# Kernel optimization log

Hardware: AMD Instinct MI355X
Metric: run time of the kernel (lower is better)

## Reference

```python
import jax, jax.numpy as jnp
import numpy as np
from jax import lax

NMODES, STEP, DTAPS, NTAPS = 2, 5, 1001, 101
HID = 100
L_FIBER = 2000000.0
DZ = L_FIBER / STEP
GAMMA = 0.0016567
D_PARAM = 16.5
FC = 299792458.0 / 1.55e-6
FS_NOM = 160e9
B, SEQ = 4, 500000


def _get_beta2(D, Fc):
    c_kms = 299792458.0 / 1e3  # speed of light [km/s]
    lamb = c_kms / Fc          # wavelength [km]
    return -(D * lamb ** 2) / (2.0 * np.pi * c_kms)


def _dispersion_kernel(Fs):
    # Fs: [B] sampling rate in Hz -> time-domain dispersion kernel [B, DTAPS] complex64
    beta2 = _get_beta2(D_PARAM, FC) / 1000.0  # [s^2/m]
    beta1 = 0.0  # Fi == Fc so the walk-off term vanishes
    dz = -DZ     # module calls dispersion_kernel(-self.dz, ...)
    f = np.fft.fftfreq(DTAPS).astype(np.float32)
    omega = 2.0 * np.pi * Fs[:, None] * f  # [B, DTAPS] rad/s
    phase = (beta2 / 2.0) * omega ** 2 * dz + beta1 * omega * dz
    kf = jnp.exp(-1j * phase)  # freq-domain response, complex64
    return jnp.fft.fftshift(jnp.fft.ifft(kf, axis=-1), axes=-1).astype(jnp.complex64)


def _nonlinear_kernel(task_info, W1, b1, W2, b2):
    # hypernetwork-generated nonlinear kernel [B, NMODES, NMODES, NTAPS]
    scale = 1.0 / 200.0
    b = task_info.shape[0]
    Fs = task_info[:, 2] / FS_NOM
    Ts = (1.0 / Fs)[:, None, None]  # [B,1,1] (broadcasts over taps like expand)
    pos = jnp.abs(jnp.arange(-(NTAPS // 2), NTAPS // 2 + 1)).astype(jnp.float32)
    pos = pos[None, :, None] * scale  # [1,NTAPS,1]
    inp = pos * Ts ** 2               # [B,NTAPS,1]
    h = jax.nn.relu(inp @ W1 + b1)    # [B,NTAPS,HID]
    mlp_out = h @ W2 + b2             # [B,NTAPS,NMODES^2]
    k1 = Ts ** 2 * mlp_out * jnp.exp(-pos * Ts ** 2)
    return jnp.transpose(k1, (0, 2, 1)).reshape(b, NMODES, NMODES, NTAPS)


def _corr(x, h):
    # x:[B,M,L] real, h:[B,taps] -> valid cross-correlation [B,M,L-taps+1] (torch conv1d semantics)
    def one(xb, hb):
        return lax.conv_general_dilated(xb[:, None, :], hb[None, None, :], (1,), 'VALID')[:, 0]
    return jax.vmap(one)(x, h)


def _nconv(p, K):
    # p:[B,Min,L], K:[B,Mout,Min,taps] -> [B,Mout,L-taps+1]
    def one(pb, Kb):
        return lax.conv_general_dilated(pb[None], Kb, (1,), 'VALID')[0]
    return jax.vmap(one)(p, K)


def _forward(x_real, x_imag, task_info, W1, b1, W2, b2):
    P = 0.001 * 10.0 ** (task_info[:, 0] / 10.0) / NMODES  # launch power per mode [W]
    Dk = _dispersion_kernel(task_info[:, 2])
    hr, hi = jnp.real(Dk), jnp.imag(Dk)
    Nk = _nonlinear_kernel(task_info, W1, b1, W2, b2)
    xr = jnp.transpose(x_real, (0, 2, 1))  # [B,M,L]
    xi = jnp.transpose(x_imag, (0, 2, 1))
    trim = (NTAPS - 1) // 2
    coef = (GAMMA * DZ) * P[:, None, None]
    for _ in range(STEP):
        # complex dispersion conv: (xr+i xi) * (hr+i hi)
        ar = _corr(xr, hr) - _corr(xi, hi)
        ai = _corr(xr, hi) + _corr(xi, hr)
        # nonlinear phase from |x|^2 filtered by hypernet kernel
        phi = _nconv(ar ** 2 + ai ** 2, Nk)  # [B,M,L-ntaps+1]
        theta = phi * coef
        c, s = jnp.cos(theta), jnp.sin(theta)
        art = ar[:, :, trim:ar.shape[2] - trim]
        ait = ai[:, :, trim:ai.shape[2] - trim]
        # x * exp(i*theta)
        xr = art * c - ait * s
        xi = art * s + ait * c
    out = jnp.stack([xr, xi], axis=-1)      # [B,M,Lout,2]
    return jnp.transpose(out, (0, 2, 1, 3))  # [B,Lout,M,2] (real/imag stacked)


def setup_inputs() -> dict:
    key = jax.random.key(0)
    k = jax.random.split(key, 6)
    x_real = jax.random.normal(k[0], (B, SEQ, NMODES), jnp.float32)
    x_imag = jax.random.normal(k[1], (B, SEQ, NMODES), jnp.float32)
    Pdbm = jax.random.uniform(k[2], (B,), jnp.float32, -2.0, 2.0)
    task_info = jnp.stack([Pdbm,
                           jnp.full((B,), FC, jnp.float32),
                           jnp.full((B,), FS_NOM, jnp.float32),
                           jnp.ones((B,), jnp.float32)], axis=1)
    W1 = jax.random.normal(k[3], (1, HID), jnp.float32) * 0.5
    b1 = jnp.zeros((HID,), jnp.float32)
    W2 = jax.random.normal(k[4], (HID, NMODES * NMODES), jnp.float32) * 0.02
    b2 = jnp.zeros((NMODES * NMODES,), jnp.float32)
    return {"x_real": x_real, "x_imag": x_imag, "task_info": task_info,
            "W1": W1, "b1": b1, "W2": W2, "b2": b2}


def reference(x_real, x_imag, task_info, W1, b1, W2, b2):
    return _forward(x_real, x_imag, task_info, W1, b1, W2, b2)
```

## Files before the change

### kernel.cpp

```cpp
#include <hip/hip_runtime.h>

#define NM      2
#define STEPS_C 5
#define DTAPS_C 1001
#define NTAPS_C 101
#define HID_C   100
#define B_C     4
#define SEQ_C   500000
#define SSTR    SEQ_C
#define NKP     104
#define FS_NOM_D 160000000000.0
#define PI_D 3.14159265358979323846

#define SWZ(L) ((L) + ((((unsigned)(L)) >> 5) << 2))

#define LD4V(A0,A1,A2,A3, SRC) { float4 q_ = *(const float4*)&(SRC); \
    A0=q_.x; A1=q_.y; A2=q_.z; A3=q_.w; }

__global__ void build_disp(const float* __restrict__ task,
                           float* __restrict__ HR, float* __restrict__ HI)
{
    __shared__ double skr[DTAPS_C], ski[DTAPS_C];
    const int b = blockIdx.y;
    const double Fs = (double)task[b * 4 + 2];
    const double c_kms = 299792458.0 / 1000.0;
    const double Fc    = 299792458.0 / 1.55e-6;
    const double lamb  = c_kms / Fc;
    const double beta2 = -(16.5 * lamb * lamb) / (2.0 * PI_D * c_kms) / 1000.0;
    const double dz    = -400000.0;

    for (int k = threadIdx.x; k < DTAPS_C; k += blockDim.x) {
        double fk = ((k <= DTAPS_C / 2) ? (double)k : (double)(k - DTAPS_C)) / (double)DTAPS_C;
        double om = 2.0 * PI_D * Fs * fk;
        double ph = 0.5 * beta2 * om * om * dz;
        ph = fmod(ph, 2.0 * PI_D);
        double s, c; sincos(ph, &s, &c);
        skr[k] = c;  ski[k] = -s;
    }
    __syncthreads();

    const int ln = threadIdx.x >> 3;
    const int kp = threadIdx.x & 7;
    const int n  = blockIdx.x * 32 + ln;
    double dr = 0.0, di = 0.0;
    {
        const int nn = (n < DTAPS_C) ? n : 0;
        const int r0 = (nn * kp) % DTAPS_C;
        const int rs = (nn * 8) % DTAPS_C;
        double a0 = 2.0 * PI_D * (double)r0 / (double)DTAPS_C;
        double as = 2.0 * PI_D * (double)rs / (double)DTAPS_C;
        double s0, c0, ss, cs;
        sincos(a0, &s0, &c0);
        sincos(as, &ss, &cs);
        for (int k = kp; k < DTAPS_C; k += 8) {
            dr += skr[k] * c0 - ski[k] * s0;
            di += skr[k] * s0 + ski[k] * c0;
            const double nc = c0 * cs - s0 * ss;
            s0 = c0 * ss + s0 * cs;
            c0 = nc;
        }
    }
    #pragma unroll
    for (int m = 1; m <= 4; m <<= 1) {
        dr += __shfl_xor(dr, m, 64);
        di += __shfl_xor(di, m, 64);
    }
    if (kp == 0 && n < DTAPS_C) {
        int m = n + DTAPS_C / 2; if (m >= DTAPS_C) m -= DTAPS_C;
        HR[b * DTAPS_C + m] = (float)(dr / (double)DTAPS_C);
        HI[b * DTAPS_C + m] = (float)(di / (double)DTAPS_C);
    }
}

__global__ void build_G(const float* __restrict__ HR, const float* __restrict__ HI,
                        float* __restrict__ Gb)
{
    __shared__ float shr[DTAPS_C], shi[DTAPS_C];
    const int b = blockIdx.y;
    for (int k = threadIdx.x; k < DTAPS_C; k += blockDim.x) {
        shr[k] = HR[b * DTAPS_C + k];
        shi[k] = HI[b * DTAPS_C + k];
    }
    __syncthreads();

    const int ln = threadIdx.x >> 3;
    const int kp = threadIdx.x & 7;
    const int f  = blockIdx.x * 32 + ln;
    double ar = 0.0, ai = 0.0;
    {
        const int r0 = (f * kp) & 4095;
        const int rs = (f * 8) & 4095;
        double a0 = (2.0 * PI_D / 4096.0) * (double)r0;
        double as = (2.0 * PI_D / 4096.0) * (double)rs;
        double s0, c0, ss, cs;
        sincos(a0, &s0, &c0);
        sincos(as, &ss, &cs);
        for (int k = kp; k < DTAPS_C; k += 8) {
            const double hre = (double)shr[k], him = (double)shi[k];
            ar += hre * c0 - him * s0;
            ai += hre * s0 + him * c0;
            const double nc = c0 * cs - s0 * ss;
            s0 = c0 * ss + s0 * cs;
            c0 = nc;
        }
    }
    #pragma unroll
    for (int m = 1; m <= 4; m <<= 1) {
        ar += __shfl_xor(ar, m, 64);
        ai += __shfl_xor(ai, m, 64);
    }
    if (kp == 0) {
        const int p = ((f & 15) << 8) + (((f >> 4) & 15) << 4) + (f >> 8);
        Gb[(size_t)(b * 4096 + p) * 2 + 0] = (float)(ar * (1.0 / 4096.0));
        Gb[(size_t)(b * 4096 + p) * 2 + 1] = (float)(ai * (1.0 / 4096.0));
    }
}

__global__ void build_nk(const float* __restrict__ task,
                         const float* __restrict__ W1, const float* __restrict__ b1,
                         const float* __restrict__ W2, const float* __restrict__ b2,
                         float* __restrict__ NKg, float* __restrict__ COEF)
{
    const int tid = threadIdx.x;
    for (int i = tid; i < B_C * 4 * NKP; i += blockDim.x) NKg[i] = 0.f;
    if (tid < B_C) {
        float pdbm = task[tid * 4 + 0];
        float P = 0.001f * powf(10.f, pdbm * 0.1f) / (float)NM;
        COEF[tid] = (float)(0.0016567 * 400000.0) * P;
    }
    __syncthreads();
    if (tid < B_C * NTAPS_C) {
        const int b = tid / NTAPS_C, tap = tid % NTAPS_C;
        float Fsn = task[b * 4 + 2] * (float)(1.0 / FS_NOM_D);
        float Ts = 1.f / Fsn, Ts2 = Ts * Ts;
        float pos = fabsf((float)(tap - NTAPS_C / 2)) * (1.f / 200.f);
        float inp = pos * Ts2;
        float o0 = b2[0], o1 = b2[1], o2 = b2[2], o3 = b2[3];
        for (int j = 0; j < HID_C; ++j) {
            float h = fmaxf(fmaf(inp, W1[j], b1[j]), 0.f);
            o0 = fmaf(h, W2[j * 4 + 0], o0);
            o1 = fmaf(h, W2[j * 4 + 1], o1);
            o2 = fmaf(h, W2[j * 4 + 2], o2);
            o3 = fmaf(h, W2[j * 4 + 3], o3);
        }
        float sc = Ts2 * expf(-pos * Ts2);
        NKg[(b * 4 + 0) * NKP + tap] = o0 * sc;
        NKg[(b * 4 + 1) * NKP + tap] = o1 * sc;
        NKg[(b * 4 + 2) * NKP + tap] = o2 * sc;
        NKg[(b * 4 + 3) * NKP + tap] = o3 * sc;
    }
}

__global__ void transpose_in(const float* __restrict__ xr_in, const float* __restrict__ xi_in,
                             float* __restrict__ XR, float* __restrict__ XI)
{
    int idx = blockIdx.x * blockDim.x + threadIdx.x;
    if (idx >= B_C * SEQ_C) return;
    int b = idx / SEQ_C, t = idx - b * SEQ_C;
    float2 vr = ((const float2*)xr_in)[idx];
    float2 vi = ((const float2*)xi_in)[idx];
    XR[(size_t)(b * 2 + 0) * SSTR + t] = vr.x;
    XR[(size_t)(b * 2 + 1) * SSTR + t] = vr.y;
    XI[(size_t)(b * 2 + 0) * SSTR + t] = vi.x;
    XI[(size_t)(b * 2 + 1) * SSTR + t] = vi.y;
}

template<int SGN>
__device__ __forceinline__ void dft4(float& ar, float& ai, float& br, float& bi,
                                     float& cr, float& ci, float& dr, float& di)
{
    float t0r = ar + cr, t0i = ai + ci;
    float t1r = ar - cr, t1i = ai - ci;
    float t2r = br + dr, t2i = bi + di;
    float t3r = br - dr, t3i = bi - di;
    ar = t0r + t2r; ai = t0i + t2i;
    cr = t0r - t2r; ci = t0i - t2i;
    if (SGN < 0) {
        br = t1r + t3i; bi = t1i - t3r;
        dr = t1r - t3i; di = t1i + t3r;
    } else {
        br = t1r - t3i; bi = t1i + t3r;
        dr = t1r + t3i; di = t1i - t3r;
    }
}

template<int SGN>
__device__ __forceinline__ void tw16(float& r, float& i, float c, float s)
{
    float nr, ni;
    if (SGN < 0) { nr = r * c + i * s; ni = i * c - r * s; }
    else         { nr = r * c - i * s; ni = i * c + r * s; }
    r = nr; i = ni;
}

template<int SGN>
__device__ __forceinline__ void dft16(float (&xr)[16], float (&xi)[16])
{
    #pragma unroll
    for (int n1 = 0; n1 < 4; ++n1)
        dft4<SGN>(xr[n1], xi[n1], xr[n1+4], xi[n1+4],
                  xr[n1+8], xi[n1+8], xr[n1+12], xi[n1+12]);
    const float C1 = 0.923879532511286756f, S1 = 0.382683432365089772f;
    const float C2 = 0.707106781186547524f;
    tw16<SGN>(xr[5],  xi[5],  C1,  S1);
    tw16<SGN>(xr[9],  xi[9],  C2,  C2);
    tw16<SGN>(xr[13], xi[13], S1,  C1);
    tw16<SGN>(xr[6],  xi[6],  C2,  C2);
    tw16<SGN>(xr[10], xi[10], 0.f, 1.f);
    tw16<SGN>(xr[14], xi[14], -C2, C2);
    tw16<SGN>(xr[7],  xi[7],  S1,  C1);
    tw16<SGN>(xr[11], xi[11], -C2, C2);
    tw16<SGN>(xr[15], xi[15], -C1, -S1);
    #pragma unroll
    for (int k4 = 0; k4 < 4; ++k4)
        dft4<SGN>(xr[4*k4+0], xi[4*k4+0], xr[4*k4+1], xi[4*k4+1],
                  xr[4*k4+2], xi[4*k4+2], xr[4*k4+3], xi[4*k4+3]);
}

#define FFTN  4096
#define FSTEP 3096
#define PH(i) ((i) + ((((unsigned)(i)) >> 5) << 1))
#define LDSN  4352

__global__ __launch_bounds__(256, 2) void disp_fft(
    const float* __restrict__ XR, const float* __restrict__ XI,
    const float* __restrict__ Gb,
    float* __restrict__ AR, float* __restrict__ AI, int La)
{
    __shared__ __align__(16) float sre[LDSN];
    __shared__ __align__(16) float sim[LDSN];
    const int t = threadIdx.x;
    const int seq = blockIdx.y;
    const int b = seq >> 1;
    const int tile0 = blockIdx.x * FSTEP;
    const int Lin = La + (DTAPS_C - 1);
    const int rem_in = Lin - tile0;
    const float* xr = XR + (size_t)seq * SSTR + tile0;
    const float* xi = XI + (size_t)seq * SSTR + tile0;

    #pragma unroll
    for (int q = 0; q < 4; ++q) {
        const int i0 = q * 1024 + t * 4;
        float4 vr4 = make_float4(0.f, 0.f, 0.f, 0.f);
        float4 vi4 = make_float4(0.f, 0.f, 0.f, 0.f);
        if (i0 + 3 < rem_in) {
            vr4 = *(const float4*)(xr + i0);
            vi4 = *(const float4*)(xi + i0);
        } else {
            if (i0 + 0 < rem_in) { vr4.x = xr[i0+0]; vi4.x = xi[i0+0]; }
            if (i0 + 1 < rem_in) { vr4.y = xr[i0+1]; vi4.y = xi[i0+1]; }
            if (i0 + 2 < rem_in) { vr4.z = xr[i0+2]; vi4.z = xi[i0+2]; }
        }
        const int p = PH(i0);
        sre[p+0] = vr4.x; sre[p+1] = vr4.y; sre[p+2] = vr4.z; sre[p+3] = vr4.w;
        sim[p+0] = vi4.x; sim[p+1] = vi4.y; sim[p+2] = vi4.z; sim[p+3] = vi4.w;
    }
    __syncthreads();

    float vr[16], vi[16];

    {
        const int base = PH(t);
        #pragma unroll
        for (int m = 0; m < 16; ++m) { vr[m] = sre[base + 272*m]; vi[m] = sim[base + 272*m]; }
        dft16<-1>(vr, vi);
        float s, c; sincosf((float)(-2.0 * PI_D / 4096.0) * (float)t, &s, &c);
        float twr = 1.f, twi = 0.f;
        #pragma unroll
        for (int k = 0; k < 16; ++k) {
            const int sl = 4*(k&3) + (k>>2);
            const float orr = vr[sl]*twr - vi[sl]*twi;
            const float oii = vr[sl]*twi + vi[sl]*twr;
            sre[base + 272*k] = orr; sim[base + 272*k] = oii;
            const float ntr = twr*c - twi*s; twi = twr*s + twi*c; twr = ntr;
        }
    }
    __syncthreads();

    {
        const int j = t & 15, blk = t >> 4;
        const int base = 272*blk + j;
        #pragma unroll
        for (int m = 0; m < 16; ++m) {
            const int o = base + 16*m + 2*(m>>1);
            vr[m] = sre[o]; vi[m] = sim[o];
        }
        dft16<-1>(vr, vi);
        float s, c; sincosf((float)(-2.0 * PI_D / 256.0) * (float)j, &s, &c);
        float twr = 1.f, twi = 0.f;
        #pragma unroll
        for (int k = 0; k < 16; ++k) {
            const int sl = 4*(k&3) + (k>>2);
            const int o = base + 16*k + 2*(k>>1);
            const float orr = vr[sl]*twr - vi[sl]*twi;
            const float oii = vr[sl]*twi + vi[sl]*twr;
            sre[o] = orr; sim[o] = oii;
            const float ntr = twr*c - twi*s; twi = twr*s + twi*c; twr = ntr;
        }
    }
    __syncthreads();

    {
        const int base = 16*t + 2*(t>>1);
        #pragma unroll
        for (int m = 0; m < 16; ++m) { vr[m] = sre[base + m]; vi[m] = sim[base + m]; }
        dft16<-1>(vr, vi);
        const float2* gp = ((const float2*)Gb) + ((size_t)b << 12) + (t << 4);
        float wr2[16], wi2[16];
        #pragma unroll
        for (int k = 0; k < 16; ++k) {
            const int sl = 4*(k&3) + (k>>2);
            const float2 g = gp[k];
            wr2[k] = vr[sl]*g.x - vi[sl]*g.y;
            wi2[k] = vr[sl]*g.y + vi[sl]*g.x;
        }
        dft16<1>(wr2, wi2);
        #pragma unroll
        for (int m = 0; m < 16; ++m) {
            const int sl = 4*(m&3) + (m>>2);
            sre[base + m] = wr2[sl]; sim[base + m] = wi2[sl];
        }
    }
    __syncthreads();

    {
        const int j = t & 15, blk = t >> 4;
        const int base = 272*blk + j;
        float s, c; sincosf((float)(2.0 * PI_D / 256.0) * (float)j, &s, &c);
        float twr = 1.f, twi = 0.f;
        #pragma unroll
        for (int k = 0; k < 16; ++k) {
            const int o = base + 16*k + 2*(k>>1);
            const float a = sre[o], d = sim[o];
            vr[k] = a*twr - d*twi; vi[k] = a*twi + d*twr;
            const float ntr = twr*c - twi*s; twi = twr*s + twi*c; twr = ntr;
        }
        dft16<1>(vr, vi);
        #pragma unroll
        for (int m = 0; m < 16; ++m) {
            const int sl = 4*(m&3) + (m>>2);
            const int o = base + 16*m + 2*(m>>1);
            sre[o] = vr[sl]; sim[o] = vi[sl];
        }
    }
    __syncthreads();

    {
        const int base = PH(t);
        float s, c; sincosf((float)(2.0 * PI_D / 4096.0) * (float)t, &s, &c);
        float twr = 1.f, twi = 0.f;
        #pragma unroll
        for (int k = 0; k < 16; ++k) {
            const float a = sre[base + 272*k], d = sim[base + 272*k];
            vr[k] = a*twr - d*twi; vi[k] = a*twi + d*twr;
            const float ntr = twr*c - twi*s; twi = twr*s + twi*c; twr = ntr;
        }
        dft16<1>(vr, vi);
        #pragma unroll
        for (int m = 0; m < 16; ++m) {
            const int sl = 4*(m&3) + (m>>2);
            sre[base + 272*m] = vr[sl]; sim[base + 272*m] = vi[sl];
        }
    }
    __syncthreads();

    const int nout = min(FSTEP, La - tile0);
    float* arp = AR + (size_t)seq * SSTR + tile0;
    float* aip = AI + (size_t)seq * SSTR + tile0;
    #pragma unroll
    for (int q = 0; q < 4; ++q) {
        const int i0 = q * 1024 + t * 4;
        if (i0 >= nout) continue;
        const int p = PH(i0);
        if (i0 + 3 < nout) {
            *(float4*)(arp + i0) = make_float4(sre[p], sre[p+1], sre[p+2], sre[p+3]);
            *(float4*)(aip + i0) = make_float4(sim[p], sim[p+1], sim[p+2], sim[p+3]);
        } else {
            for (int k = 0; k < 4; ++k) if (i0 + k < nout) {
                arp[i0+k] = sre[p+k]; aip[i0+k] = sim[p+k];
            }
        }
    }
}

#define K2_BLOCK 256
#define K2_TILE  2048
#define K2_LDSL  2176
#define K2_LDSP  2448

#define N_CH8(W_, V_, N_, P0, P1, KK)                                      \
  {                                                                        \
    LD4V(N_[0],N_[1],N_[2],N_[3], sp[P0]);                                 \
    LD4V(N_[4],N_[5],N_[6],N_[7], sp[P1]);                                 \
    _Pragma("unroll")                                                      \
    for (int d = 0; d < 8; ++d) {                                          \
      const float av = nkA[(KK) + d], bv = nkB[(KK) + d];                  \
      _Pragma("unroll")                                                    \
      for (int j = 0; j < 8; ++j) {                                        \
        const float xv = (j + d < 8) ? W_[j + d] : V_[j + d - 8];          \
        th0[j] = fmaf(av, xv, th0[j]);                                     \
        th1[j] = fmaf(bv, xv, th1[j]);                                     \
      }                                                                    \
    }                                                                      \
  }

__global__ __launch_bounds__(K2_BLOCK, 4) void nl_rotate(
    const float* __restrict__ AR, const float* __restrict__ AI,
    const float* __restrict__ NKg, const float* __restrict__ COEF,
    float* __restrict__ XR, float* __restrict__ XI,
    float* __restrict__ OUT, int Lb, int finalstep)
{
    __shared__ __align__(16) float sp0[K2_LDSP];
    __shared__ __align__(16) float sp1[K2_LDSP];
    const int b = blockIdx.y;
    const int tile0 = blockIdx.x * K2_TILE;
    const int nout  = min(K2_TILE, Lb - tile0);
    const int cnt   = nout + NTAPS_C - 1;
    const float* ar0 = AR + (size_t)(2 * b + 0) * SSTR + tile0;
    const float* ai0 = AI + (size_t)(2 * b + 0) * SSTR + tile0;
    const float* ar1 = AR + (size_t)(2 * b + 1) * SSTR + tile0;
    const float* ai1 = AI + (size_t)(2 * b + 1) * SSTR + tile0;

    for (int i = threadIdx.x; i < K2_LDSL; i += K2_BLOCK) {
        float p0 = 0.f, p1 = 0.f;
        if (i < cnt) {
            float a = ar0[i], c = ai0[i];
            float d = ar1[i], e = ai1[i];
            p0 = fmaf(a, a, c * c);
            p1 = fmaf(d, d, e * e);
        }
        const int p = SWZ(i);
        sp0[p] = p0; sp1[p] = p1;
    }
    __syncthreads();

    const int t0 = threadIdx.x * 8;
    if (t0 >= nout) return;

    float th0[8], th1[8];
    #pragma unroll
    for (int j = 0; j < 8; ++j) { th0[j] = 0.f; th1[j] = 0.f; }
    const float* nkb = NKg + b * 4 * NKP;

    const int a0 = SWZ(t0 + 16), a1 = SWZ(t0 + 20), a2 = SWZ(t0 + 24), a3 = SWZ(t0 + 28);
    const int a4 = SWZ(t0 + 32), a5 = SWZ(t0 + 36), a6 = SWZ(t0 + 40), a7 = SWZ(t0 + 44);

    for (int im = 0; im < 2; ++im) {
        const float* sp  = im ? sp1 : sp0;
        const float* nkA = nkb + (0 * 2 + im) * NKP;
        const float* nkB = nkb + (1 * 2 + im) * NKP;
        float U[8], V[8], N[8];
        LD4V(U[0],U[1],U[2],U[3], sp[SWZ(t0)]);
        LD4V(U[4],U[5],U[6],U[7], sp[SWZ(t0 + 4)]);
        LD4V(V[0],V[1],V[2],V[3], sp[SWZ(t0 + 8)]);
        LD4V(V[4],V[5],V[6],V[7], sp[SWZ(t0 + 12)]);
        N_CH8(U, V, N, a0,       a1,        0);
        N_CH8(V, N, U, a2,       a3,        8);
        N_CH8(N, U, V, a4,       a5,       16);
        N_CH8(U, V, N, a6,       a7,       24);
        N_CH8(V, N, U, a0 + 36,  a1 + 36,  32);
        N_CH8(N, U, V, a2 + 36,  a3 + 36,  40);
        N_CH8(U, V, N, a4 + 36,  a5 + 36,  48);
        N_CH8(V, N, U, a6 + 36,  a7 + 36,  56);
        N_CH8(N, U, V, a0 + 72,  a1 + 72,  64);
        N_CH8(U, V, N, a2 + 72,  a3 + 72,  72);
        N_CH8(V, N, U, a4 + 72,  a5 + 72,  80);
        N_CH8(N, U, V, a6 + 72,  a7 + 72,  88);
        N_CH8(U, V, N, a0 + 108, a1 + 108, 96);
    }

    const float coef = COEF[b];
    const int tg = tile0 + t0;
    const float* art0 = ar0 + t0 + NTAPS_C / 2;
    const float* ait0 = ai0 + t0 + NTAPS_C / 2;
    const float* art1 = ar1 + t0 + NTAPS_C / 2;
    const float* ait1 = ai1 + t0 + NTAPS_C / 2;

    float or0[8], oi0[8], or1[8], oi1[8];
    #pragma unroll
    for (int j = 0; j < 8; ++j) {
        float s0, c0, s1, c1;
        sincosf(th0[j] * coef, &s0, &c0);
        sincosf(th1[j] * coef, &s1, &c1);
        float a0v = art0[j], b0v = ait0[j];
        float a1v = art1[j], b1v = ait1[j];
        or0[j] = fmaf(a0v, c0, -b0v * s0);
        oi0[j] = fmaf(a0v, s0,  b0v * c0);
        or1[j] = fmaf(a1v, c1, -b1v * s1);
        oi1[j] = fmaf(a1v, s1,  b1v * c1);
    }

    const int rem = nout - t0;
    if (finalstep) {
        float4* op = (float4*)(OUT + (size_t)(b * Lb + tg) * 4);
        if (rem >= 8) {
            #pragma unroll
            for (int j = 0; j < 8; ++j) op[j] = make_float4(or0[j], oi0[j], or1[j], oi1[j]);
        } else {
            for (int j = 0; j < rem; ++j) op[j] = make_float4(or0[j], oi0[j], or1[j], oi1[j]);
        }
    } else {
        float* xr0 = XR + (size_t)(2 * b + 0) * SSTR + tg;
        float* xi0 = XI + (size_t)(2 * b + 0) * SSTR + tg;
        float* xr1 = XR + (size_t)(2 * b + 1) * SSTR + tg;
        float* xi1 = XI + (size_t)(2 * b + 1) * SSTR + tg;
        if (rem >= 8) {
            ((float4*)xr0)[0] = make_float4(or0[0], or0[1], or0[2], or0[3]);
            ((float4*)xr0)[1] = make_float4(or0[4], or0[5], or0[6], or0[7]);
            ((float4*)xi0)[0] = make_float4(oi0[0], oi0[1], oi0[2], oi0[3]);
            ((float4*)xi0)[1] = make_float4(oi0[4], oi0[5], oi0[6], oi0[7]);
            ((float4*)xr1)[0] = make_float4(or1[0], or1[1], or1[2], or1[3]);
            ((float4*)xr1)[1] = make_float4(or1[4], or1[5], or1[6], or1[7]);
            ((float4*)xi1)[0] = make_float4(oi1[0], oi1[1], oi1[2], oi1[3]);
            ((float4*)xi1)[1] = make_float4(oi1[4], oi1[5], oi1[6], oi1[7]);
        } else {
            for (int j = 0; j < rem; ++j) {
                xr0[j] = or0[j]; xi0[j] = oi0[j];
                xr1[j] = or1[j]; xi1[j] = oi1[j];
            }
        }
    }
}

extern "C" void kernel_launch(void* const* d_in, const int* in_sizes, int n_in,
                              void* d_out, int out_size, void* d_ws, size_t ws_size,
                              hipStream_t stream)
{
    const float* x_real = (const float*)d_in[0];
    const float* x_imag = (const float*)d_in[1];
    const float* task   = (const float*)d_in[2];
    const float* W1     = (const float*)d_in[3];
    const float* b1     = (const float*)d_in[4];
    const float* W2     = (const float*)d_in[5];
    const float* b2     = (const float*)d_in[6];
    float* out = (float*)d_out;
    float* ws  = (float*)d_ws;

    float* HR   = ws;
    float* HI   = HR + B_C * DTAPS_C;
    float* NKg  = HI + B_C * DTAPS_C;
    float* COEF = NKg + B_C * 4 * NKP;
    float* Gb   = ws + 16384;
    float* XR = ws + 16384 + 32768;
    float* XI = XR + (size_t)B_C * 2 * SEQ_C;
    float* AR = XI + (size_t)B_C * 2 * SEQ_C;
    float* AI = AR + (size_t)B_C * 2 * SEQ_C;

    build_disp<<<dim3(32, B_C), 256, 0, stream>>>(task, HR, HI);
    build_nk<<<1, 512, 0, stream>>>(task, W1, b1, W2, b2, NKg, COEF);
    build_G<<<dim3(128, B_C), 256, 0, stream>>>(HR, HI, Gb);
    {
        int n = B_C * SEQ_C;
        transpose_in<<<(n + 255) / 256, 256, 0, stream>>>(x_real, x_imag, XR, XI);
    }

    int L = SEQ_C;
    for (int s = 0; s < STEPS_C; ++s) {
        const int La = L - (DTAPS_C - 1);
        const int Lb = La - (NTAPS_C - 1);
        dim3 g1((La + FSTEP - 1) / FSTEP, B_C * NM);
        disp_fft<<<g1, 256, 0, stream>>>(XR, XI, Gb, AR, AI, La);
        dim3 g2((Lb + K2_TILE - 1) / K2_TILE, B_C);
        nl_rotate<<<g2, K2_BLOCK, 0, stream>>>(AR, AI, NKg, COEF, XR, XI, out,
                                               Lb, (s == STEPS_C - 1) ? 1 : 0);
        L = Lb;
    }
}
```

Measured before the change: 348.0 us.

## Fuse dispersion FFT and nonlinear rotation into one per-step kernel

Merges the dispersion FFT-convolution kernel and the nonlinear phase-rotation kernel into a single dbp_step kernel. Each block FFT-filters both modes for a tile, computes power directly into LDS and keeps the linear output in registers. This removes the global round-trip of the intermediate AR/AI arrays, and the step input and output now ping-pong between two buffers. In exchange each block handles both modes serially, uses more LDS, and the per-thread output grows to 12 samples, which raises register pressure and lowers the count of useful outputs per FFT tile (2996 vs 3096).

Measured after the change: 671.4 us. 92.9% more time.

```diff
diff --git a/kernel.cpp b/kernel.cpp
--- a/kernel.cpp
+++ b/kernel.cpp
@@ -218,45 +218,12 @@
 }
 
 #define FFTN  4096
-#define FSTEP 3096
 #define PH(i) ((i) + ((((unsigned)(i)) >> 5) << 1))
 #define LDSN  4352
 
-__global__ __launch_bounds__(256, 2) void disp_fft(
-    const float* __restrict__ XR, const float* __restrict__ XI,
-    const float* __restrict__ Gb,
-    float* __restrict__ AR, float* __restrict__ AI, int La)
-{
-    __shared__ __align__(16) float sre[LDSN];
-    __shared__ __align__(16) float sim[LDSN];
-    const int t = threadIdx.x;
-    const int seq = blockIdx.y;
-    const int b = seq >> 1;
-    const int tile0 = blockIdx.x * FSTEP;
-    const int Lin = La + (DTAPS_C - 1);
-    const int rem_in = Lin - tile0;
-    const float* xr = XR + (size_t)seq * SSTR + tile0;
-    const float* xi = XI + (size_t)seq * SSTR + tile0;
-
-    #pragma unroll
-    for (int q = 0; q < 4; ++q) {
-        const int i0 = q * 1024 + t * 4;
-        float4 vr4 = make_float4(0.f, 0.f, 0.f, 0.f);
-        float4 vi4 = make_float4(0.f, 0.f, 0.f, 0.f);
-        if (i0 + 3 < rem_in) {
-            vr4 = *(const float4*)(xr + i0);
-            vi4 = *(const float4*)(xi + i0);
-        } else {
-            if (i0 + 0 < rem_in) { vr4.x = xr[i0+0]; vi4.x = xi[i0+0]; }
-            if (i0 + 1 < rem_in) { vr4.y = xr[i0+1]; vi4.y = xi[i0+1]; }
-            if (i0 + 2 < rem_in) { vr4.z = xr[i0+2]; vi4.z = xi[i0+2]; }
-        }
-        const int p = PH(i0);
-        sre[p+0] = vr4.x; sre[p+1] = vr4.y; sre[p+2] = vr4.z; sre[p+3] = vr4.w;
-        sim[p+0] = vi4.x; sim[p+1] = vi4.y; sim[p+2] = vi4.z; sim[p+3] = vi4.w;
-    }
-    __syncthreads();
-
+__device__ __forceinline__ void fft_conv_4096(float* sre, float* sim,
+                                              const int t, const float2* gp)
+{
     float vr[16], vi[16];
 
     {
@@ -305,7 +272,6 @@
         #pragma unroll
         for (int m = 0; m < 16; ++m) { vr[m] = sre[base + m]; vi[m] = sim[base + m]; }
         dft16<-1>(vr, vi);
-        const float2* gp = ((const float2*)Gb) + ((size_t)b << 12) + (t << 4);
         float wr2[16], wi2[16];
         #pragma unroll
         for (int k = 0; k < 16; ++k) {
@@ -363,156 +329,182 @@
         }
     }
     __syncthreads();
-
-    const int nout = min(FSTEP, La - tile0);
-    float* arp = AR + (size_t)seq * SSTR + tile0;
-    float* aip = AI + (size_t)seq * SSTR + tile0;
-    #pragma unroll
-    for (int q = 0; q < 4; ++q) {
-        const int i0 = q * 1024 + t * 4;
-        if (i0 >= nout) continue;
-        const int p = PH(i0);
-        if (i0 + 3 < nout) {
-            *(float4*)(arp + i0) = make_float4(sre[p], sre[p+1], sre[p+2], sre[p+3]);
-            *(float4*)(aip + i0) = make_float4(sim[p], sim[p+1], sim[p+2], sim[p+3]);
-        } else {
-            for (int k = 0; k < 4; ++k) if (i0 + k < nout) {
-                arp[i0+k] = sre[p+k]; aip[i0+k] = sim[p+k];
-            }
-        }
-    }
-}
-
-#define K2_BLOCK 256
-#define K2_TILE  2048
-#define K2_LDSL  2176
-#define K2_LDSP  2448
-
-#define N_CH8(W_, V_, N_, P0, P1, KK)                                      \
+}
+
+#define NOUTB 2996
+#define PLOG  3120
+#define PPHYS 3520
+
+#define C12(A_,B_,C_,D_, P0, P1, KK)                                       \
   {                                                                        \
-    LD4V(N_[0],N_[1],N_[2],N_[3], sp[P0]);                                 \
-    LD4V(N_[4],N_[5],N_[6],N_[7], sp[P1]);                                 \
+    LD4V(D_[0],D_[1],D_[2],D_[3], sp[P0]);                                 \
+    LD4V(D_[4],D_[5],D_[6],D_[7], sp[P1]);                                 \
     _Pragma("unroll")                                                      \
     for (int d = 0; d < 8; ++d) {                                          \
       const float av = nkA[(KK) + d], bv = nkB[(KK) + d];                  \
       _Pragma("unroll")                                                    \
-      for (int j = 0; j < 8; ++j) {                                        \
-        const float xv = (j + d < 8) ? W_[j + d] : V_[j + d - 8];          \
+      for (int j = 0; j < 12; ++j) {                                       \
+        const float xv = (j + d < 8) ? A_[j + d]                           \
+                       : ((j + d < 16) ? B_[j + d - 8] : C_[j + d - 16]);  \
         th0[j] = fmaf(av, xv, th0[j]);                                     \
         th1[j] = fmaf(bv, xv, th1[j]);                                     \
       }                                                                    \
     }                                                                      \
   }
 
-__global__ __launch_bounds__(K2_BLOCK, 4) void nl_rotate(
-    const float* __restrict__ AR, const float* __restrict__ AI,
+#define CONVBODY                                                           \
+  {                                                                        \
+    float A_[8], B_[8], C_[8], D_[8];                                      \
+    LD4V(A_[0],A_[1],A_[2],A_[3], sp[SWZ(t0)]);                            \
+    LD4V(A_[4],A_[5],A_[6],A_[7], sp[SWZ(t0 + 4)]);                        \
+    LD4V(B_[0],B_[1],B_[2],B_[3], sp[SWZ(t0 + 8)]);                        \
+    LD4V(B_[4],B_[5],B_[6],B_[7], sp[SWZ(t0 + 12)]);                       \
+    LD4V(C_[0],C_[1],C_[2],C_[3], sp[SWZ(t0 + 16)]);                       \
+    LD4V(C_[4],C_[5],C_[6],C_[7], sp[SWZ(t0 + 20)]);                       \
+    C12(A_,B_,C_,D_, q0,      q1,       0);                                \
+    C12(B_,C_,D_,A_, q2,      q3,       8);                                \
+    C12(C_,D_,A_,B_, q4,      q5,      16);                                \
+    C12(D_,A_,B_,C_, q6,      q7,      24);                                \
+    C12(A_,B_,C_,D_, q0 + 36, q1 + 36, 32);                                \
+    C12(B_,C_,D_,A_, q2 + 36, q3 + 36, 40);                                \
+    C12(C_,D_,A_,B_, q4 + 36, q5 + 36, 48);                                \
+    C12(D_,A_,B_,C_, q6 + 36, q7 + 36, 56);                                \
+    C12(A_,B_,C_,D_, q0 + 72, q1 + 72, 64);                                \
+    C12(B_,C_,D_,A_, q2 + 72, q3 + 72, 72);                                \
+    C12(C_,D_,A_,B_, q4 + 72, q5 + 72, 80);                                \
+    C12(D_,A_,B_,C_, q6 + 72, q7 + 72, 88);                                \
+    C12(A_,B_,C_,D_, q0 + 108,q1 + 108,96);                                \
+  }
+
+__global__ __launch_bounds__(256, 2) void dbp_step(
+    const float* __restrict__ INR, const float* __restrict__ INI,
+    const float* __restrict__ Gb,
     const float* __restrict__ NKg, const float* __restrict__ COEF,
-    float* __restrict__ XR, float* __restrict__ XI,
+    float* __restrict__ OUTR, float* __restrict__ OUTI,
     float* __restrict__ OUT, int Lb, int finalstep)
 {
-    __shared__ __align__(16) float sp0[K2_LDSP];
-    __shared__ __align__(16) float sp1[K2_LDSP];
-    const int b = blockIdx.y;
-    const int tile0 = blockIdx.x * K2_TILE;
-    const int nout  = min(K2_TILE, Lb - tile0);
-    const int cnt   = nout + NTAPS_C - 1;
-    const float* ar0 = AR + (size_t)(2 * b + 0) * SSTR + tile0;
-    const float* ai0 = AI + (size_t)(2 * b + 0) * SSTR + tile0;
-    const float* ar1 = AR + (size_t)(2 * b + 1) * SSTR + tile0;
-    const float* ai1 = AI + (size_t)(2 * b + 1) * SSTR + tile0;
-
-    for (int i = threadIdx.x; i < K2_LDSL; i += K2_BLOCK) {
-        float p0 = 0.f, p1 = 0.f;
-        if (i < cnt) {
-            float a = ar0[i], c = ai0[i];
-            float d = ar1[i], e = ai1[i];
-            p0 = fmaf(a, a, c * c);
-            p1 = fmaf(d, d, e * e);
-        }
-        const int p = SWZ(i);
-        sp0[p] = p0; sp1[p] = p1;
-    }
-    __syncthreads();
-
-    const int t0 = threadIdx.x * 8;
+    __shared__ __align__(16) float sre[LDSN];
+    __shared__ __align__(16) float sim[LDSN];
+    __shared__ __align__(16) float pw0[PPHYS];
+    __shared__ __align__(16) float pw1[PPHYS];
+    const int t  = threadIdx.x;
+    const int b  = blockIdx.y;
+    const int tile0 = blockIdx.x * NOUTB;
+    const int nout  = min(NOUTB, Lb - tile0);
+    const int Lin   = Lb + (DTAPS_C - 1) + (NTAPS_C - 1);
+    const int rem_in = Lin - tile0;
+    const float2* gp = ((const float2*)Gb) + ((size_t)b << 12) + (t << 4);
+    const int t0 = t * 12;
+
+    float rar0[12], rai0[12], rar1[12], rai1[12];
+
+    auto do_mode = [&](const float* __restrict__ xr, const float* __restrict__ xi,
+                       float* __restrict__ pw, float (&rar)[12], float (&rai)[12]) {
+        #pragma unroll
+        for (int q = 0; q < 4; ++q) {
+            const int i0 = q * 1024 + t * 4;
+            float4 vr4 = make_float4(0.f, 0.f, 0.f, 0.f);
+            float4 vi4 = make_float4(0.f, 0.f, 0.f, 0.f);
+            if (i0 + 3 < rem_in) {
+                vr4 = *(const float4*)(xr + i0);
+                vi4 = *(const float4*)(xi + i0);
+            } else {
+                if (i0 + 0 < rem_in) { vr4.x = xr[i0+0]; vi4.x = xi[i0+0]; }
+                if (i0 + 1 < rem_in) { vr4.y = xr[i0+1]; vi4.y = xi[i0+1]; }
+                if (i0 + 2 < rem_in) { vr4.z = xr[i0+2]; vi4.z = xi[i0+2]; }
+            }
+            const int p = PH(i0);
+            sre[p+0] = vr4.x; sre[p+1] = vr4.y; sre[p+2] = vr4.z; sre[p+3] = vr4.w;
+            sim[p+0] = vi4.x; sim[p+1] = vi4.y; sim[p+2] = vi4.z; sim[p+3] = vi4.w;
+        }
+        __syncthreads();
+
+        fft_conv_4096(sre, sim, t, gp);
+
+        #pragma unroll
+        for (int q = 0; q < 4; ++q) {
+            const int i0 = q * 1024 + t * 4;
+            if (i0 < PLOG) {
+                const int ph = PH(i0), sw = SWZ(i0);
+                #pragma unroll
+                for (int u = 0; u < 4; ++u) {
+                    const float ar = sre[ph + u], ai = sim[ph + u];
+                    pw[sw + u] = fmaf(ar, ar, ai * ai);
+                }
+            }
+        }
+        #pragma unroll
+        for (int u = 0; u < 12; ++u) {
+            const int ph = PH(t0 + 50 + u);
+            rar[u] = sre[ph]; rai[u] = sim[ph];
+        }
+        __syncthreads();
+    };
+
+    do_mode(INR + (size_t)(2*b + 0) * SSTR + tile0,
+            INI + (size_t)(2*b + 0) * SSTR + tile0, pw0, rar0, rai0);
+    do_mode(INR + (size_t)(2*b + 1) * SSTR + tile0,
+            INI + (size_t)(2*b + 1) * SSTR + tile0, pw1, rar1, rai1);
+
     if (t0 >= nout) return;
 
-    float th0[8], th1[8];
+    float th0[12], th1[12];
     #pragma unroll
-    for (int j = 0; j < 8; ++j) { th0[j] = 0.f; th1[j] = 0.f; }
+    for (int j = 0; j < 12; ++j) { th0[j] = 0.f; th1[j] = 0.f; }
     const float* nkb = NKg + b * 4 * NKP;
 
-    const int a0 = SWZ(t0 + 16), a1 = SWZ(t0 + 20), a2 = SWZ(t0 + 24), a3 = SWZ(t0 + 28);
-    const int a4 = SWZ(t0 + 32), a5 = SWZ(t0 + 36), a6 = SWZ(t0 + 40), a7 = SWZ(t0 + 44);
-
-    for (int im = 0; im < 2; ++im) {
-        const float* sp  = im ? sp1 : sp0;
-        const float* nkA = nkb + (0 * 2 + im) * NKP;
-        const float* nkB = nkb + (1 * 2 + im) * NKP;
-        float U[8], V[8], N[8];
-        LD4V(U[0],U[1],U[2],U[3], sp[SWZ(t0)]);
-        LD4V(U[4],U[5],U[6],U[7], sp[SWZ(t0 + 4)]);
-        LD4V(V[0],V[1],V[2],V[3], sp[SWZ(t0 + 8)]);
-        LD4V(V[4],V[5],V[6],V[7], sp[SWZ(t0 + 12)]);
-        N_CH8(U, V, N, a0,       a1,        0);
-        N_CH8(V, N, U, a2,       a3,        8);
-        N_CH8(N, U, V, a4,       a5,       16);
-        N_CH8(U, V, N, a6,       a7,       24);
-        N_CH8(V, N, U, a0 + 36,  a1 + 36,  32);
-        N_CH8(N, U, V, a2 + 36,  a3 + 36,  40);
-        N_CH8(U, V, N, a4 + 36,  a5 + 36,  48);
-        N_CH8(V, N, U, a6 + 36,  a7 + 36,  56);
-        N_CH8(N, U, V, a0 + 72,  a1 + 72,  64);
-        N_CH8(U, V, N, a2 + 72,  a3 + 72,  72);
-        N_CH8(V, N, U, a4 + 72,  a5 + 72,  80);
-        N_CH8(N, U, V, a6 + 72,  a7 + 72,  88);
-        N_CH8(U, V, N, a0 + 108, a1 + 108, 96);
+    const int q0 = SWZ(t0 + 24), q1 = SWZ(t0 + 28), q2 = SWZ(t0 + 32), q3 = SWZ(t0 + 36);
+    const int q4 = SWZ(t0 + 40), q5 = SWZ(t0 + 44), q6 = SWZ(t0 + 48), q7 = SWZ(t0 + 52);
+
+    {
+        const float* sp  = pw0;
+        const float* nkA = nkb + 0 * NKP;
+        const float* nkB = nkb + 2 * NKP;
+        CONVBODY
+    }
+    {
+        const float* sp  = pw1;
+        const float* nkA = nkb + 1 * NKP;
+        const float* nkB = nkb + 3 * NKP;
+        CONVBODY
     }
 
     const float coef = COEF[b];
-    const int tg = tile0 + t0;
-    const float* art0 = ar0 + t0 + NTAPS_C / 2;
-    const float* ait0 = ai0 + t0 + NTAPS_C / 2;
-    const float* art1 = ar1 + t0 + NTAPS_C / 2;
-    const float* ait1 = ai1 + t0 + NTAPS_C / 2;
-
-    float or0[8], oi0[8], or1[8], oi1[8];
+    float or0[12], oi0[12], or1[12], oi1[12];
     #pragma unroll
-    for (int j = 0; j < 8; ++j) {
+    for (int j = 0; j < 12; ++j) {
         float s0, c0, s1, c1;
         sincosf(th0[j] * coef, &s0, &c0);
         sincosf(th1[j] * coef, &s1, &c1);
-        float a0v = art0[j], b0v = ait0[j];
-        float a1v = art1[j], b1v = ait1[j];
-        or0[j] = fmaf(a0v, c0, -b0v * s0);
-        oi0[j] = fmaf(a0v, s0,  b0v * c0);
-        or1[j] = fmaf(a1v, c1, -b1v * s1);
-        oi1[j] = fmaf(a1v, s1,  b1v * c1);
-    }
-
+        or0[j] = fmaf(rar0[j], c0, -rai0[j] * s0);
+        oi0[j] = fmaf(rar0[j], s0,  rai0[j] * c0);
+        or1[j] = fmaf(rar1[j], c1, -rai1[j] * s1);
+        oi1[j] = fmaf(rar1[j], s1,  rai1[j] * c1);
+    }
+
+    const int tg  = tile0 + t0;
     const int rem = nout - t0;
     if (finalstep) {
         float4* op = (float4*)(OUT + (size_t)(b * Lb + tg) * 4);
-        if (rem >= 8) {
+        if (rem >= 12) {
             #pragma unroll
-            for (int j = 0; j < 8; ++j) op[j] = make_float4(or0[j], oi0[j], or1[j], oi1[j]);
+            for (int j = 0; j < 12; ++j) op[j] = make_float4(or0[j], oi0[j], or1[j], oi1[j]);
         } else {
             for (int j = 0; j < rem; ++j) op[j] = make_float4(or0[j], oi0[j], or1[j], oi1[j]);
         }
     } else {
-        float* xr0 = XR + (size_t)(2 * b + 0) * SSTR + tg;
-        float* xi0 = XI + (size_t)(2 * b + 0) * SSTR + tg;
-        float* xr1 = XR + (size_t)(2 * b + 1) * SSTR + tg;
-        float* xi1 = XI + (size_t)(2 * b + 1) * SSTR + tg;
-        if (rem >= 8) {
-            ((float4*)xr0)[0] = make_float4(or0[0], or0[1], or0[2], or0[3]);
-            ((float4*)xr0)[1] = make_float4(or0[4], or0[5], or0[6], or0[7]);
-            ((float4*)xi0)[0] = make_float4(oi0[0], oi0[1], oi0[2], oi0[3]);
-            ((float4*)xi0)[1] = make_float4(oi0[4], oi0[5], oi0[6], oi0[7]);
-            ((float4*)xr1)[0] = make_float4(or1[0], or1[1], or1[2], or1[3]);
-            ((float4*)xr1)[1] = make_float4(or1[4], or1[5], or1[6], or1[7]);
-            ((float4*)xi1)[0] = make_float4(oi1[0], oi1[1], oi1[2], oi1[3]);
-            ((float4*)xi1)[1] = make_float4(oi1[4], oi1[5], oi1[6], oi1[7]);
+        float* xr0 = OUTR + (size_t)(2*b + 0) * SSTR + tg;
+        float* xi0 = OUTI + (size_t)(2*b + 0) * SSTR + tg;
+        float* xr1 = OUTR + (size_t)(2*b + 1) * SSTR + tg;
+        float* xi1 = OUTI + (size_t)(2*b + 1) * SSTR + tg;
+        if (rem >= 12) {
+            #pragma unroll
+            for (int w = 0; w < 3; ++w) {
+                ((float4*)xr0)[w] = make_float4(or0[4*w], or0[4*w+1], or0[4*w+2], or0[4*w+3]);
+                ((float4*)xi0)[w] = make_float4(oi0[4*w], oi0[4*w+1], oi0[4*w+2], oi0[4*w+3]);
+                ((float4*)xr1)[w] = make_float4(or1[4*w], or1[4*w+1], or1[4*w+2], or1[4*w+3]);
+                ((float4*)xi1)[w] = make_float4(oi1[4*w], oi1[4*w+1], oi1[4*w+2], oi1[4*w+3]);
+            }
         } else {
             for (int j = 0; j < rem; ++j) {
                 xr0[j] = or0[j]; xi0[j] = oi0[j];
@@ -543,8 +535,8 @@
     float* Gb   = ws + 16384;
     float* XR = ws + 16384 + 32768;
     float* XI = XR + (size_t)B_C * 2 * SEQ_C;
-    float* AR = XI + (size_t)B_C * 2 * SEQ_C;
-    float* AI = AR + (size_t)B_C * 2 * SEQ_C;
+    float* YR = XI + (size_t)B_C * 2 * SEQ_C;
+    float* YI = YR + (size_t)B_C * 2 * SEQ_C;
 
     build_disp<<<dim3(32, B_C), 256, 0, stream>>>(task, HR, HI);
     build_nk<<<1, 512, 0, stream>>>(task, W1, b1, W2, b2, NKg, COEF);
@@ -555,14 +547,14 @@
     }
 
     int L = SEQ_C;
+    float *inR = XR, *inI = XI, *outR = YR, *outI = YI;
     for (int s = 0; s < STEPS_C; ++s) {
-        const int La = L - (DTAPS_C - 1);
-        const int Lb = La - (NTAPS_C - 1);
-        dim3 g1((La + FSTEP - 1) / FSTEP, B_C * NM);
-        disp_fft<<<g1, 256, 0, stream>>>(XR, XI, Gb, AR, AI, La);
-        dim3 g2((Lb + K2_TILE - 1) / K2_TILE, B_C);
-        nl_rotate<<<g2, K2_BLOCK, 0, stream>>>(AR, AI, NKg, COEF, XR, XI, out,
-                                               Lb, (s == STEPS_C - 1) ? 1 : 0);
+        const int Lb = L - (DTAPS_C - 1) - (NTAPS_C - 1);
+        dim3 g((Lb + NOUTB - 1) / NOUTB, B_C);
+        dbp_step<<<g, 256, 0, stream>>>(inR, inI, Gb, NKg, COEF, outR, outI, out,
+                                        Lb, (s == STEPS_C - 1) ? 1 : 0);
+        float* tr = inR; inR = outR; outR = tr;
+        float* ti = inI; inI = outI; outI = ti;
         L = Lb;
     }
 }
```
